# Optimization experiments

Hardware: AMD Instinct MI355X
Metric: run time of the kernel (lower is better)

The kernel has to match this reference:

```python
import jax, jax.numpy as jnp
import numpy as np

EPS = 1e-12  # F.normalize default eps


def setup_inputs() -> dict:
    key = jax.random.key(0)
    ks = jax.random.split(key, 8)
    b, c, h, w = 8, 192, 128, 128
    s = 0.02
    return {
        "x_in": jax.random.normal(ks[0], (b, c, h, w), dtype=jnp.float32),
        "w_split": jax.random.normal(ks[1], (c, c), dtype=jnp.float32) * s,
        "w_q": jax.random.normal(ks[2], (c, c), dtype=jnp.float32) * s,
        "w_k": jax.random.normal(ks[3], (c, c), dtype=jnp.float32) * s,
        "w_v": jax.random.normal(ks[4], (c, c), dtype=jnp.float32) * s,
        "w_proj": jax.random.normal(ks[5], (c, c), dtype=jnp.float32) * s,
        "b_proj": jax.random.normal(ks[6], (c,), dtype=jnp.float32) * s,
        "w_out": jax.random.normal(ks[7], (c, c), dtype=jnp.float32) * s,
    }


def _l2norm(x):
    # F.normalize(p=2, dim=-1): x / max(||x||, eps)
    n = jnp.sqrt(jnp.sum(x * x, axis=-1, keepdims=True))
    return x / jnp.maximum(n, EPS)


def reference(x_in, w_split, w_q, w_k, w_v, w_proj, b_proj, w_out):
    b, c, h, w = x_in.shape
    # conv_split0: 1x1 conv, no bias -> channel matmul
    x = jnp.einsum('oc,bchw->bohw', w_split, x_in)
    # [b,h,w,c] -> [b,hw,c]
    x = x.transpose(0, 2, 3, 1).reshape(b, h * w, c)
    # Linear: y = x @ W^T
    q = jnp.einsum('bnc,oc->bon', x, w_q)  # [b,c,hw] (already transposed)
    k = jnp.einsum('bnc,oc->bon', x, w_k)
    v = jnp.einsum('bnc,oc->bon', x, w_v)
    q = _l2norm(q)
    k = _l2norm(k)
    attn = jax.nn.softmax(jnp.einsum('bcn,bdn->bcd', k, q), axis=-1)  # [b,c,c]
    y = jnp.einsum('bcd,bdn->bcn', attn, v)  # [b,c,hw]
    y = y.transpose(0, 2, 1)  # [b,hw,c]
    out = jnp.einsum('bnc,oc->bno', y, w_proj) + b_proj
    out = out.reshape(b, h, w, c).transpose(0, 3, 1, 2)  # [b,c,h,w]
    out = jnp.einsum('oc,bchw->bohw', w_out, out)
    return out
```

## Files before the change

### kernel.cpp

```cpp
#include <hip/hip_runtime.h>


static constexpr int B_ = 8;
static constexpr int C_ = 192;
static constexpr int N_ = 16384;
static constexpr int CC2 = C_ * C_;
static constexpr int NCHUNK = 32;

using u16x8 = __attribute__((ext_vector_type(8))) unsigned short;
using bf16x8 = __attribute__((ext_vector_type(8))) __bf16;
using f32x4 = __attribute__((ext_vector_type(4))) float;

__device__ __forceinline__ unsigned short f2bf(float f) {
  unsigned int u = __builtin_bit_cast(unsigned int, f);
  u += 0x7FFFu + ((u >> 16) & 1u);
  return (unsigned short)(u >> 16);
}

__device__ __forceinline__ f32x4 mfma16(u16x8 a, u16x8 b, f32x4 c) {
  return __builtin_amdgcn_mfma_f32_16x16x32_bf16(
      __builtin_bit_cast(bf16x8, a), __builtin_bit_cast(bf16x8, b), c, 0, 0, 0);
}

__global__ void fold_kernel(const float* __restrict__ wsplit, const float* __restrict__ wq,
                            const float* __restrict__ wk, const float* __restrict__ wv,
                            const float* __restrict__ wproj, const float* __restrict__ bproj,
                            const float* __restrict__ wout,
                            float* __restrict__ Wq, float* __restrict__ WqT,
                            float* __restrict__ Wk, float* __restrict__ Wv,
                            float* __restrict__ Wo2, float* __restrict__ bias2) {
  int idx = blockIdx.x * 256 + threadIdx.x;
  if (idx < C_) {
    float s = 0.f;
    for (int c = 0; c < C_; ++c) s += wout[idx * C_ + c] * bproj[c];
    bias2[idx] = s;
  }
  if (idx >= 4 * CC2) return;
  int which = idx / CC2;
  int rem = idx % CC2;
  int o = rem / C_, c = rem % C_;
  const float* A = (which == 0) ? wq : (which == 1) ? wk : (which == 2) ? wv : wout;
  const float* Bm = (which == 3) ? wproj : wsplit;
  float s = 0.f;
  for (int e = 0; e < C_; ++e) s += A[o * C_ + e] * Bm[e * C_ + c];
  if (which == 0) { Wq[rem] = s; WqT[c * C_ + o] = s; }
  else if (which == 1) Wk[rem] = s;
  else if (which == 2) Wv[rem] = s;
  else Wo2[rem] = s;
}

template <bool ATOMIC>
__global__ __launch_bounds__(384) void gram3_kernel(const float* __restrict__ xin,
                                                    float* __restrict__ dst) {
  const int b = blockIdx.z, half = blockIdx.y, ch = blockIdx.x;
  const int k0 = ch * 512;
  __shared__ unsigned short Xs[2][C_][72];
  const int tid = threadIdx.x;
  const int wv = tid >> 6;
  const int lane = tid & 63;
  const int ln = lane & 15, mq = lane >> 4;
  const int arow0 = half * 96 + wv * 16;
  const int cbase = tid >> 4;
  const int k4 = tid & 15;
  const float* xb = xin + (size_t)b * C_ * N_;

  f32x4 acc[12];
#pragma unroll
  for (int j = 0; j < 12; ++j) acc[j] = (f32x4)0.0f;

  float4 ld[8];
  auto load_stage = [&](int kbase) {
#pragma unroll
    for (int j = 0; j < 8; ++j)
      ld[j] = *(const float4*)(xb + (size_t)(j * 24 + cbase) * N_ + kbase + k4 * 4);
  };
  auto write_stage = [&](int buf) {
#pragma unroll
    for (int j = 0; j < 8; ++j) {
      unsigned int lo = (unsigned)f2bf(ld[j].x) | ((unsigned)f2bf(ld[j].y) << 16);
      unsigned int hi = (unsigned)f2bf(ld[j].z) | ((unsigned)f2bf(ld[j].w) << 16);
      uint2 pk; pk.x = lo; pk.y = hi;
      *(uint2*)&Xs[buf][j * 24 + cbase][k4 * 4] = pk;
    }
  };

  load_stage(k0);
  write_stage(0);
  __syncthreads();
  for (int s = 0; s < 8; ++s) {
    if (s < 7) load_stage(k0 + (s + 1) * 64);
    const int cb = s & 1;
#pragma unroll
    for (int ks = 0; ks < 2; ++ks) {
      const int kk = ks * 32 + mq * 8;
      u16x8 a0 = *(const u16x8*)&Xs[cb][arow0 + ln][kk];
#pragma unroll
      for (int ct = 0; ct < 12; ++ct) {
        u16x8 bf = *(const u16x8*)&Xs[cb][ct * 16 + ln][kk];
        acc[ct] = mfma16(a0, bf, acc[ct]);
      }
    }
    if (s < 7) {
      write_stage(cb ^ 1);
      __syncthreads();
    }
  }
  float* out = ATOMIC ? dst + (size_t)b * CC2
                      : dst + ((size_t)b * NCHUNK + ch) * CC2;
#pragma unroll
  for (int ct = 0; ct < 12; ++ct)
#pragma unroll
    for (int r = 0; r < 4; ++r) {
      int row = arow0 + mq * 4 + r;
      int col = ct * 16 + ln;
      if (ATOMIC) atomicAdd(&out[row * C_ + col], acc[ct][r]);
      else out[row * C_ + col] = acc[ct][r];
    }
}

__global__ void gsum_kernel(const float* __restrict__ P, float* __restrict__ G) {
  const int j = (blockIdx.x * 256 + threadIdx.x) * 4;
  const int b = blockIdx.y;
  const float* base = P + (size_t)b * NCHUNK * CC2 + j;
  float4 s = {0.f, 0.f, 0.f, 0.f};
#pragma unroll
  for (int ch = 0; ch < NCHUNK; ++ch) {
    float4 v = *(const float4*)(base + (size_t)ch * CC2);
    s.x += v.x; s.y += v.y; s.z += v.z; s.w += v.w;
  }
  *(float4*)(G + (size_t)b * CC2 + j) = s;
}

__global__ __launch_bounds__(192) void tkqn_kernel(const float* __restrict__ Wk,
                                                   const float* __restrict__ Wq,
                                                   const float* __restrict__ G,
                                                   float* __restrict__ Tk,
                                                   float* __restrict__ qn) {
  const int b = blockIdx.y, d = blockIdx.x, t = threadIdx.x;
  const float* Gb = G + (size_t)b * CC2;
  float sk = 0.f, sq = 0.f;
  for (int c = 0; c < C_; ++c) {
    float g = Gb[c * C_ + t];
    sk += Wk[d * C_ + c] * g;
    sq += Wq[d * C_ + c] * g;
  }
  Tk[((size_t)b * C_ + d) * C_ + t] = sk;
  float val = sq * Wq[d * C_ + t];
  __shared__ float red[256];
  red[t] = val;
  if (t < 64) red[192 + t] = 0.f;
  __syncthreads();
  for (int st = 128; st > 0; st >>= 1) {
    if (t < st) red[t] += red[t + st];
    __syncthreads();
  }
  if (t == 0) qn[b * C_ + d] = fmaxf(sqrtf(fmaxf(red[0], 0.f)), 1e-12f);
}

__global__ __launch_bounds__(192) void attn_av_kernel(const float* __restrict__ Tk,
                                                      const float* __restrict__ WqT,
                                                      const float* __restrict__ Wk,
                                                      const float* __restrict__ Wv,
                                                      const float* __restrict__ qn,
                                                      float* __restrict__ Tv) {
  const int b = blockIdx.y, cc = blockIdx.x, t = threadIdx.x;
  __shared__ float tkrow[C_];
  __shared__ float arow[C_];
  __shared__ float red[256];
  tkrow[t] = Tk[((size_t)b * C_ + cc) * C_ + t];
  red[t] = tkrow[t] * Wk[cc * C_ + t];
  if (t < 64) red[192 + t] = 0.f;
  __syncthreads();
  for (int st = 128; st > 0; st >>= 1) {
    if (t < st) red[t] += red[t + st];
    __syncthreads();
  }
  float knv = fmaxf(sqrtf(fmaxf(red[0], 0.f)), 1e-12f);
  __syncthreads();
  float s = 0.f;
  for (int c = 0; c < C_; ++c) s += tkrow[c] * WqT[c * C_ + t];
  float lg = s / (knv * qn[b * C_ + t]);
  red[t] = lg;
  if (t < 64) red[192 + t] = -1e30f;
  __syncthreads();
  for (int st = 128; st > 0; st >>= 1) {
    if (t < st) red[t] = fmaxf(red[t], red[t + st]);
    __syncthreads();
  }
  float mx = red[0];
  __syncthreads();
  float e = expf(lg - mx);
  red[t] = e;
  if (t < 64) red[192 + t] = 0.f;
  __syncthreads();
  for (int st = 128; st > 0; st >>= 1) {
    if (t < st) red[t] += red[t + st];
    __syncthreads();
  }
  float a = e / red[0];
  arow[t] = a;
  __syncthreads();
  float sv = 0.f;
  for (int c = 0; c < C_; ++c) sv += arow[c] * Wv[c * C_ + t];
  Tv[((size_t)b * C_ + cc) * C_ + t] = sv;
}

__global__ void m_kernel(const float* __restrict__ Wo2, const float* __restrict__ Tv,
                         float* __restrict__ Mout) {
  int idx = blockIdx.x * 256 + threadIdx.x;
  if (idx >= B_ * CC2) return;
  int b = idx / CC2;
  int rc = idx % CC2;
  int i = rc / C_, j = rc % C_;
  float s = 0.f;
  for (int c = 0; c < C_; ++c) s += Wo2[i * C_ + c] * Tv[((size_t)b * C_ + c) * C_ + j];
  Mout[idx] = s;
}

__global__ __launch_bounds__(384) void final2_kernel(const float* __restrict__ xin,
                                                     const float* __restrict__ Mw,
                                                     const float* __restrict__ bias2,
                                                     float* __restrict__ out) {
  const int b = blockIdx.y;
  const int p0 = blockIdx.x * 128;
  __shared__ unsigned short Ts[128 * 192];
  const int tid = threadIdx.x;
  const int wv = tid >> 6;
  const int lane = tid & 63;
  const int ln = lane & 15, mq = lane >> 4;
  const float* Mb = Mw + (size_t)b * CC2;

  u16x8 afr[6][2];
  float bo[2][4];
#pragma unroll
  for (int i = 0; i < 2; ++i) {
    int row = 32 * wv + 16 * i + ln;
#pragma unroll
    for (int kc = 0; kc < 6; ++kc) {
      const float* src = Mb + row * C_ + kc * 32 + mq * 8;
      float4 u0 = *(const float4*)(src);
      float4 u1 = *(const float4*)(src + 4);
      u16x8 a;
      a[0] = f2bf(u0.x); a[1] = f2bf(u0.y); a[2] = f2bf(u0.z); a[3] = f2bf(u0.w);
      a[4] = f2bf(u1.x); a[5] = f2bf(u1.y); a[6] = f2bf(u1.z); a[7] = f2bf(u1.w);
      afr[kc][i] = a;
    }
#pragma unroll
    for (int r = 0; r < 4; ++r) bo[i][r] = bias2[32 * wv + 16 * i + mq * 4 + r];
  }

#pragma unroll
  for (int j = 0; j < 16; ++j) {
    int lin = j * 384 + tid;
    int c = lin >> 5, p4 = lin & 31;
    float4 v = *(const float4*)(xin + ((size_t)b * C_ + c) * N_ + p0 + p4 * 4);
#pragma unroll
    for (int jj = 0; jj < 4; ++jj) {
      int e = (jj + (p4 >> 1)) & 3;
      float val = (e == 0) ? v.x : (e == 1) ? v.y : (e == 2) ? v.z : v.w;
      int p = p4 * 4 + e;
      int idx = p * 192 + ((((c >> 3) ^ (p & 7)) << 3) | (c & 7));
      Ts[idx] = f2bf(val);
    }
  }
  __syncthreads();

#pragma unroll
  for (int pt = 0; pt < 8; ++pt) {
    const int p = pt * 16 + ln;
    f32x4 acc0 = (f32x4)0.0f, acc1 = (f32x4)0.0f;
#pragma unroll
    for (int kc = 0; kc < 6; ++kc) {
      u16x8 bf = *(const u16x8*)&Ts[p * 192 + (((kc * 4 + mq) ^ (p & 7)) << 3)];
      acc0 = mfma16(afr[kc][0], bf, acc0);
      acc1 = mfma16(afr[kc][1], bf, acc1);
    }
#pragma unroll
    for (int r = 0; r < 4; ++r) {
      int row0 = 32 * wv + mq * 4 + r;
      int row1 = row0 + 16;
      int pp = p0 + pt * 16 + ln;
      out[((size_t)b * C_ + row0) * N_ + pp] = acc0[r] + bo[0][r];
      out[((size_t)b * C_ + row1) * N_ + pp] = acc1[r] + bo[1][r];
    }
  }
}

extern "C" void kernel_launch(void* const* d_in, const int* in_sizes, int n_in,
                              void* d_out, int out_size, void* d_ws, size_t ws_size,
                              hipStream_t stream) {
  const float* xin    = (const float*)d_in[0];
  const float* wsplit = (const float*)d_in[1];
  const float* wq     = (const float*)d_in[2];
  const float* wk     = (const float*)d_in[3];
  const float* wv     = (const float*)d_in[4];
  const float* wproj  = (const float*)d_in[5];
  const float* bproj  = (const float*)d_in[6];
  const float* wout   = (const float*)d_in[7];
  float* out = (float*)d_out;

  float* ws = (float*)d_ws;
  float* G     = ws;
  float* Wq    = G + (size_t)B_ * CC2;
  float* WqT   = Wq + CC2;
  float* Wk    = WqT + CC2;
  float* Wv    = Wk + CC2;
  float* Wo2   = Wv + CC2;
  float* bias2 = Wo2 + CC2;
  float* Tk    = bias2 + 256;
  float* Tv    = Tk + (size_t)B_ * CC2;
  float* Mw    = Tv + (size_t)B_ * CC2;
  float* qn    = Mw + (size_t)B_ * CC2;
  float* P     = qn + 256 * B_;

  size_t base_floats = (size_t)(P - ws);
  size_t need_bytes = (base_floats + (size_t)B_ * NCHUNK * CC2) * sizeof(float);
  bool use_partials = ws_size >= need_bytes;

  fold_kernel<<<(4 * CC2 + 255) / 256, 256, 0, stream>>>(
      wsplit, wq, wk, wv, wproj, bproj, wout, Wq, WqT, Wk, Wv, Wo2, bias2);
  if (use_partials) {
    gram3_kernel<false><<<dim3(NCHUNK, 2, B_), 384, 0, stream>>>(xin, P);
    gsum_kernel<<<dim3(CC2 / 1024, B_), 256, 0, stream>>>(P, G);
  } else {
    hipMemsetAsync(G, 0, (size_t)B_ * CC2 * sizeof(float), stream);
    gram3_kernel<true><<<dim3(NCHUNK, 2, B_), 384, 0, stream>>>(xin, G);
  }
  tkqn_kernel<<<dim3(C_, B_), 192, 0, stream>>>(Wk, Wq, G, Tk, qn);
  attn_av_kernel<<<dim3(C_, B_), 192, 0, stream>>>(Tk, WqT, Wk, Wv, qn, Tv);
  m_kernel<<<(B_ * CC2 + 255) / 256, 256, 0, stream>>>(Wo2, Tv, Mw);
  final2_kernel<<<dim3(N_ / 128, B_), 384, 0, stream>>>(xin, Mw, bias2, out);
}
```

Before: 323.7 us.

## Merge small kernels, switch gram to 32x32 MFMA, pipeline final projection

The gram kernel now uses 32x32x16 MFMA with 192-thread blocks. The weight-fold work is merged into the partial-sum reduction kernel, and the three small attention kernels are fused into one cooperative kernel that uses grid syncs. The final kernel now processes four pixel tiles per block with double-buffered LDS so that global loads overlap MFMA work. The goal is to cut launch overhead and raise MFMA efficiency, at the cost of the grid-sync overhead and co-residency requirements of a 1536-block cooperative launch.

After: 644.9 us. 1.99x slower.

```diff
diff --git a/kernel.cpp b/kernel.cpp
--- a/kernel.cpp
+++ b/kernel.cpp
@@ -1,4 +1,8 @@
 #include <hip/hip_runtime.h>
+#include <hip/hip_bf16.h>
+#include <hip/hip_cooperative_groups.h>
+
+namespace cg = cooperative_groups;
 
 
 static constexpr int B_ = 8;
@@ -10,35 +14,129 @@
 using u16x8 = __attribute__((ext_vector_type(8))) unsigned short;
 using bf16x8 = __attribute__((ext_vector_type(8))) __bf16;
 using f32x4 = __attribute__((ext_vector_type(4))) float;
+using f32x16 = __attribute__((ext_vector_type(16))) float;
 
 __device__ __forceinline__ unsigned short f2bf(float f) {
   unsigned int u = __builtin_bit_cast(unsigned int, f);
   u += 0x7FFFu + ((u >> 16) & 1u);
   return (unsigned short)(u >> 16);
 }
-
+__device__ __forceinline__ unsigned int pk2bf(float x, float y) {
+  return (unsigned)f2bf(x) | ((unsigned)f2bf(y) << 16);
+}
 __device__ __forceinline__ f32x4 mfma16(u16x8 a, u16x8 b, f32x4 c) {
   return __builtin_amdgcn_mfma_f32_16x16x32_bf16(
       __builtin_bit_cast(bf16x8, a), __builtin_bit_cast(bf16x8, b), c, 0, 0, 0);
 }
-
-__global__ void fold_kernel(const float* __restrict__ wsplit, const float* __restrict__ wq,
-                            const float* __restrict__ wk, const float* __restrict__ wv,
-                            const float* __restrict__ wproj, const float* __restrict__ bproj,
-                            const float* __restrict__ wout,
-                            float* __restrict__ Wq, float* __restrict__ WqT,
-                            float* __restrict__ Wk, float* __restrict__ Wv,
-                            float* __restrict__ Wo2, float* __restrict__ bias2) {
-  int idx = blockIdx.x * 256 + threadIdx.x;
+__device__ __forceinline__ f32x16 mfma32(u16x8 a, u16x8 b, f32x16 c) {
+  return __builtin_amdgcn_mfma_f32_32x32x16_bf16(
+      __builtin_bit_cast(bf16x8, a), __builtin_bit_cast(bf16x8, b), c, 0, 0, 0);
+}
+
+template <bool PART>
+__global__ __launch_bounds__(192, 2) void gram4_kernel(const float* __restrict__ xin,
+                                                       float* __restrict__ dst) {
+  const int b = blockIdx.z, half = blockIdx.y, ch = blockIdx.x;
+  const int k0 = ch * 512;
+  __shared__ unsigned short Xs[2][C_][72];
+  const int tid = threadIdx.x;
+  const int wv = tid >> 6;
+  const int lane = tid & 63;
+  const int m32 = lane & 31;
+  const int hi = lane >> 5;
+  const int arow0 = half * 96 + wv * 32;
+  const int cth = tid >> 4;
+  const int k4 = tid & 15;
+  const float* xb = xin + (size_t)b * C_ * N_;
+
+  f32x16 acc[6];
+#pragma unroll
+  for (int j = 0; j < 6; ++j) acc[j] = (f32x16)0.0f;
+
+  float4 ld[16];
+  auto load_stage = [&](int kbase) {
+#pragma unroll
+    for (int j = 0; j < 16; ++j)
+      ld[j] = *(const float4*)(xb + (size_t)(j * 12 + cth) * N_ + kbase + k4 * 4);
+  };
+  auto write_stage = [&](int buf) {
+#pragma unroll
+    for (int j = 0; j < 16; ++j) {
+      uint2 pk;
+      pk.x = pk2bf(ld[j].x, ld[j].y);
+      pk.y = pk2bf(ld[j].z, ld[j].w);
+      *(uint2*)&Xs[buf][j * 12 + cth][k4 * 4] = pk;
+    }
+  };
+
+  load_stage(k0);
+  write_stage(0);
+  __syncthreads();
+  for (int s = 0; s < 8; ++s) {
+    if (s < 7) load_stage(k0 + (s + 1) * 64);
+    const int cb = s & 1;
+#pragma unroll
+    for (int ks = 0; ks < 4; ++ks) {
+      const int koff = ks * 16 + hi * 8;
+      u16x8 a = *(const u16x8*)&Xs[cb][arow0 + m32][koff];
+#pragma unroll
+      for (int ct = 0; ct < 6; ++ct) {
+        u16x8 bb = *(const u16x8*)&Xs[cb][ct * 32 + m32][koff];
+        acc[ct] = mfma32(a, bb, acc[ct]);
+      }
+    }
+    if (s < 7) {
+      write_stage(cb ^ 1);
+      __syncthreads();
+    }
+  }
+  float* outp = PART ? dst + ((size_t)b * NCHUNK + ch) * CC2
+                     : dst + (size_t)b * CC2;
+#pragma unroll
+  for (int ct = 0; ct < 6; ++ct)
+#pragma unroll
+    for (int reg = 0; reg < 16; ++reg) {
+      int row = arow0 + (reg & 3) + 8 * (reg >> 2) + 4 * hi;
+      int col = ct * 32 + m32;
+      if (PART) outp[row * C_ + col] = acc[ct][reg];
+      else atomicAdd(&outp[row * C_ + col], acc[ct][reg]);
+    }
+}
+
+__global__ void gsumfold_kernel(const float* __restrict__ P, float* __restrict__ G,
+                                const float* __restrict__ wsplit, const float* __restrict__ wq,
+                                const float* __restrict__ wk, const float* __restrict__ wv,
+                                const float* __restrict__ wproj, const float* __restrict__ bproj,
+                                const float* __restrict__ wout,
+                                float* __restrict__ Wq, float* __restrict__ WqT,
+                                float* __restrict__ Wk, float* __restrict__ Wv,
+                                float* __restrict__ Wo2, float* __restrict__ bias2,
+                                int do_gsum) {
+  const int gx = blockIdx.x, tid = threadIdx.x;
+  if (gx < 288) {
+    if (!do_gsum) return;
+    const int b = gx / 36, jb = gx % 36;
+    const int j = (jb * 256 + tid) * 4;
+    const float* base = P + (size_t)b * NCHUNK * CC2 + j;
+    float4 s = {0.f, 0.f, 0.f, 0.f};
+#pragma unroll
+    for (int ch = 0; ch < NCHUNK; ++ch) {
+      float4 v = *(const float4*)(base + (size_t)ch * CC2);
+      s.x += v.x; s.y += v.y; s.z += v.z; s.w += v.w;
+    }
+    *(float4*)(G + (size_t)b * CC2 + j) = s;
+    return;
+  }
+  const int idx = (gx - 288) * 256 + tid;
   if (idx < C_) {
     float s = 0.f;
     for (int c = 0; c < C_; ++c) s += wout[idx * C_ + c] * bproj[c];
     bias2[idx] = s;
   }
   if (idx >= 4 * CC2) return;
-  int which = idx / CC2;
-  int rem = idx % CC2;
-  int o = rem / C_, c = rem % C_;
+  const int which = idx / CC2;
+  const int rem = idx % CC2;
+  const int o = rem / C_, c = rem % C_;
   const float* A = (which == 0) ? wq : (which == 1) ? wk : (which == 2) ? wv : wout;
   const float* Bm = (which == 3) ? wproj : wsplit;
   float s = 0.f;
@@ -49,186 +147,83 @@
   else Wo2[rem] = s;
 }
 
-template <bool ATOMIC>
-__global__ __launch_bounds__(384) void gram3_kernel(const float* __restrict__ xin,
-                                                    float* __restrict__ dst) {
-  const int b = blockIdx.z, half = blockIdx.y, ch = blockIdx.x;
-  const int k0 = ch * 512;
-  __shared__ unsigned short Xs[2][C_][72];
-  const int tid = threadIdx.x;
-  const int wv = tid >> 6;
-  const int lane = tid & 63;
-  const int ln = lane & 15, mq = lane >> 4;
-  const int arow0 = half * 96 + wv * 16;
-  const int cbase = tid >> 4;
-  const int k4 = tid & 15;
-  const float* xb = xin + (size_t)b * C_ * N_;
-
-  f32x4 acc[12];
-#pragma unroll
-  for (int j = 0; j < 12; ++j) acc[j] = (f32x4)0.0f;
-
-  float4 ld[8];
-  auto load_stage = [&](int kbase) {
-#pragma unroll
-    for (int j = 0; j < 8; ++j)
-      ld[j] = *(const float4*)(xb + (size_t)(j * 24 + cbase) * N_ + kbase + k4 * 4);
-  };
-  auto write_stage = [&](int buf) {
-#pragma unroll
-    for (int j = 0; j < 8; ++j) {
-      unsigned int lo = (unsigned)f2bf(ld[j].x) | ((unsigned)f2bf(ld[j].y) << 16);
-      unsigned int hi = (unsigned)f2bf(ld[j].z) | ((unsigned)f2bf(ld[j].w) << 16);
-      uint2 pk; pk.x = lo; pk.y = hi;
-      *(uint2*)&Xs[buf][j * 24 + cbase][k4 * 4] = pk;
-    }
-  };
-
-  load_stage(k0);
-  write_stage(0);
-  __syncthreads();
-  for (int s = 0; s < 8; ++s) {
-    if (s < 7) load_stage(k0 + (s + 1) * 64);
-    const int cb = s & 1;
-#pragma unroll
-    for (int ks = 0; ks < 2; ++ks) {
-      const int kk = ks * 32 + mq * 8;
-      u16x8 a0 = *(const u16x8*)&Xs[cb][arow0 + ln][kk];
-#pragma unroll
-      for (int ct = 0; ct < 12; ++ct) {
-        u16x8 bf = *(const u16x8*)&Xs[cb][ct * 16 + ln][kk];
-        acc[ct] = mfma16(a0, bf, acc[ct]);
-      }
-    }
-    if (s < 7) {
-      write_stage(cb ^ 1);
-      __syncthreads();
-    }
-  }
-  float* out = ATOMIC ? dst + (size_t)b * CC2
-                      : dst + ((size_t)b * NCHUNK + ch) * CC2;
-#pragma unroll
-  for (int ct = 0; ct < 12; ++ct)
-#pragma unroll
-    for (int r = 0; r < 4; ++r) {
-      int row = arow0 + mq * 4 + r;
-      int col = ct * 16 + ln;
-      if (ATOMIC) atomicAdd(&out[row * C_ + col], acc[ct][r]);
-      else out[row * C_ + col] = acc[ct][r];
-    }
-}
-
-__global__ void gsum_kernel(const float* __restrict__ P, float* __restrict__ G) {
-  const int j = (blockIdx.x * 256 + threadIdx.x) * 4;
-  const int b = blockIdx.y;
-  const float* base = P + (size_t)b * NCHUNK * CC2 + j;
-  float4 s = {0.f, 0.f, 0.f, 0.f};
-#pragma unroll
-  for (int ch = 0; ch < NCHUNK; ++ch) {
-    float4 v = *(const float4*)(base + (size_t)ch * CC2);
-    s.x += v.x; s.y += v.y; s.z += v.z; s.w += v.w;
-  }
-  *(float4*)(G + (size_t)b * CC2 + j) = s;
-}
-
-__global__ __launch_bounds__(192) void tkqn_kernel(const float* __restrict__ Wk,
-                                                   const float* __restrict__ Wq,
-                                                   const float* __restrict__ G,
-                                                   float* __restrict__ Tk,
-                                                   float* __restrict__ qn) {
-  const int b = blockIdx.y, d = blockIdx.x, t = threadIdx.x;
+__device__ __forceinline__ float block_sum192(float v, float* wred, int t) {
+#pragma unroll
+  for (int off = 32; off > 0; off >>= 1) v += __shfl_down(v, off);
+  if ((t & 63) == 0) wred[t >> 6] = v;
+  __syncthreads();
+  float r = wred[0] + wred[1] + wred[2];
+  __syncthreads();
+  return r;
+}
+__device__ __forceinline__ float block_max192(float v, float* wred, int t) {
+#pragma unroll
+  for (int off = 32; off > 0; off >>= 1) v = fmaxf(v, __shfl_down(v, off));
+  if ((t & 63) == 0) wred[t >> 6] = v;
+  __syncthreads();
+  float r = fmaxf(fmaxf(wred[0], wred[1]), wred[2]);
+  __syncthreads();
+  return r;
+}
+
+__global__ __launch_bounds__(192) void mid_kernel(const float* __restrict__ G,
+                                                  const float* __restrict__ Wq,
+                                                  const float* __restrict__ WqT,
+                                                  const float* __restrict__ Wk,
+                                                  const float* __restrict__ Wv,
+                                                  const float* __restrict__ Wo2,
+                                                  float* __restrict__ qn,
+                                                  float* __restrict__ Tv,
+                                                  float* __restrict__ Mw) {
+  cg::grid_group grid = cg::this_grid();
+  const int b = blockIdx.y, r = blockIdx.x, t = threadIdx.x;
   const float* Gb = G + (size_t)b * CC2;
-  float sk = 0.f, sq = 0.f;
-  for (int c = 0; c < C_; ++c) {
-    float g = Gb[c * C_ + t];
-    sk += Wk[d * C_ + c] * g;
-    sq += Wq[d * C_ + c] * g;
-  }
-  Tk[((size_t)b * C_ + d) * C_ + t] = sk;
-  float val = sq * Wq[d * C_ + t];
-  __shared__ float red[256];
-  red[t] = val;
-  if (t < 64) red[192 + t] = 0.f;
-  __syncthreads();
-  for (int st = 128; st > 0; st >>= 1) {
-    if (t < st) red[t] += red[t + st];
-    __syncthreads();
-  }
-  if (t == 0) qn[b * C_ + d] = fmaxf(sqrtf(fmaxf(red[0], 0.f)), 1e-12f);
-}
-
-__global__ __launch_bounds__(192) void attn_av_kernel(const float* __restrict__ Tk,
-                                                      const float* __restrict__ WqT,
-                                                      const float* __restrict__ Wk,
-                                                      const float* __restrict__ Wv,
-                                                      const float* __restrict__ qn,
-                                                      float* __restrict__ Tv) {
-  const int b = blockIdx.y, cc = blockIdx.x, t = threadIdx.x;
-  __shared__ float tkrow[C_];
-  __shared__ float arow[C_];
-  __shared__ float red[256];
-  tkrow[t] = Tk[((size_t)b * C_ + cc) * C_ + t];
-  red[t] = tkrow[t] * Wk[cc * C_ + t];
-  if (t < 64) red[192 + t] = 0.f;
-  __syncthreads();
-  for (int st = 128; st > 0; st >>= 1) {
-    if (t < st) red[t] += red[t + st];
-    __syncthreads();
-  }
-  float knv = fmaxf(sqrtf(fmaxf(red[0], 0.f)), 1e-12f);
-  __syncthreads();
-  float s = 0.f;
-  for (int c = 0; c < C_; ++c) s += tkrow[c] * WqT[c * C_ + t];
-  float lg = s / (knv * qn[b * C_ + t]);
-  red[t] = lg;
-  if (t < 64) red[192 + t] = -1e30f;
-  __syncthreads();
-  for (int st = 128; st > 0; st >>= 1) {
-    if (t < st) red[t] = fmaxf(red[t], red[t + st]);
-    __syncthreads();
-  }
-  float mx = red[0];
-  __syncthreads();
+  __shared__ float sh[C_];
+  __shared__ float wred[4];
+
+  float sq = 0.f;
+  for (int c = 0; c < C_; ++c) sq += Wq[r * C_ + c] * Gb[c * C_ + t];
+  float tot = block_sum192(sq * Wq[r * C_ + t], wred, t);
+  if (t == 0) qn[b * C_ + r] = fmaxf(sqrtf(fmaxf(tot, 0.f)), 1e-12f);
+  grid.sync();
+
+  float tk = 0.f;
+  for (int c = 0; c < C_; ++c) tk += Wk[r * C_ + c] * Gb[c * C_ + t];
+  sh[t] = tk;
+  float kn2 = block_sum192(tk * Wk[r * C_ + t], wred, t);
+  float knv = fmaxf(sqrtf(fmaxf(kn2, 0.f)), 1e-12f);
+  float lg = 0.f;
+  for (int c = 0; c < C_; ++c) lg += sh[c] * WqT[c * C_ + t];
+  lg /= (knv * qn[b * C_ + t]);
+  float mx = block_max192(lg, wred, t);
   float e = expf(lg - mx);
-  red[t] = e;
-  if (t < 64) red[192 + t] = 0.f;
-  __syncthreads();
-  for (int st = 128; st > 0; st >>= 1) {
-    if (t < st) red[t] += red[t + st];
-    __syncthreads();
-  }
-  float a = e / red[0];
-  arow[t] = a;
+  float se = block_sum192(e, wred, t);
+  float a = e / se;
+  sh[t] = a;
   __syncthreads();
   float sv = 0.f;
-  for (int c = 0; c < C_; ++c) sv += arow[c] * Wv[c * C_ + t];
-  Tv[((size_t)b * C_ + cc) * C_ + t] = sv;
-}
-
-__global__ void m_kernel(const float* __restrict__ Wo2, const float* __restrict__ Tv,
-                         float* __restrict__ Mout) {
-  int idx = blockIdx.x * 256 + threadIdx.x;
-  if (idx >= B_ * CC2) return;
-  int b = idx / CC2;
-  int rc = idx % CC2;
-  int i = rc / C_, j = rc % C_;
-  float s = 0.f;
-  for (int c = 0; c < C_; ++c) s += Wo2[i * C_ + c] * Tv[((size_t)b * C_ + c) * C_ + j];
-  Mout[idx] = s;
-}
-
-__global__ __launch_bounds__(384) void final2_kernel(const float* __restrict__ xin,
+  for (int c = 0; c < C_; ++c) sv += sh[c] * Wv[c * C_ + t];
+  Tv[((size_t)b * C_ + r) * C_ + t] = sv;
+  grid.sync();
+
+  float sm = 0.f;
+  for (int c = 0; c < C_; ++c) sm += Wo2[r * C_ + c] * Tv[((size_t)b * C_ + c) * C_ + t];
+  Mw[((size_t)b * C_ + r) * C_ + t] = sm;
+}
+
+__global__ __launch_bounds__(384) void final3_kernel(const float* __restrict__ xin,
                                                      const float* __restrict__ Mw,
                                                      const float* __restrict__ bias2,
                                                      float* __restrict__ out) {
-  const int b = blockIdx.y;
-  const int p0 = blockIdx.x * 128;
-  __shared__ unsigned short Ts[128 * 192];
+  const int beta = blockIdx.x;
+  const int b = beta >> 5, q = beta & 31;
+  __shared__ unsigned short Ts[2][128 * 192];
   const int tid = threadIdx.x;
   const int wv = tid >> 6;
   const int lane = tid & 63;
   const int ln = lane & 15, mq = lane >> 4;
   const float* Mb = Mw + (size_t)b * CC2;
+  const float* xb = xin + (size_t)b * C_ * N_;
 
   u16x8 afr[6][2];
   float bo[2][4];
@@ -249,39 +244,56 @@
     for (int r = 0; r < 4; ++r) bo[i][r] = bias2[32 * wv + 16 * i + mq * 4 + r];
   }
 
-#pragma unroll
-  for (int j = 0; j < 16; ++j) {
-    int lin = j * 384 + tid;
-    int c = lin >> 5, p4 = lin & 31;
-    float4 v = *(const float4*)(xin + ((size_t)b * C_ + c) * N_ + p0 + p4 * 4);
-#pragma unroll
-    for (int jj = 0; jj < 4; ++jj) {
-      int e = (jj + (p4 >> 1)) & 3;
-      float val = (e == 0) ? v.x : (e == 1) ? v.y : (e == 2) ? v.z : v.w;
-      int p = p4 * 4 + e;
-      int idx = p * 192 + ((((c >> 3) ^ (p & 7)) << 3) | (c & 7));
-      Ts[idx] = f2bf(val);
-    }
-  }
-  __syncthreads();
-
-#pragma unroll
-  for (int pt = 0; pt < 8; ++pt) {
-    const int p = pt * 16 + ln;
-    f32x4 acc0 = (f32x4)0.0f, acc1 = (f32x4)0.0f;
-#pragma unroll
-    for (int kc = 0; kc < 6; ++kc) {
-      u16x8 bf = *(const u16x8*)&Ts[p * 192 + (((kc * 4 + mq) ^ (p & 7)) << 3)];
-      acc0 = mfma16(afr[kc][0], bf, acc0);
-      acc1 = mfma16(afr[kc][1], bf, acc1);
-    }
-#pragma unroll
-    for (int r = 0; r < 4; ++r) {
-      int row0 = 32 * wv + mq * 4 + r;
-      int row1 = row0 + 16;
-      int pp = p0 + pt * 16 + ln;
-      out[((size_t)b * C_ + row0) * N_ + pp] = acc0[r] + bo[0][r];
-      out[((size_t)b * C_ + row1) * N_ + pp] = acc1[r] + bo[1][r];
+  float4 ld[16];
+  auto load_tile = [&](int it) {
+    const int p0 = (q * 4 + it) * 128;
+#pragma unroll
+    for (int j = 0; j < 16; ++j) {
+      int lin = j * 384 + tid;
+      int c = lin >> 5, p4 = lin & 31;
+      ld[j] = *(const float4*)(xb + (size_t)c * N_ + p0 + p4 * 4);
+    }
+  };
+  auto stage = [&](int buf) {
+#pragma unroll
+    for (int j = 0; j < 16; ++j) {
+      int lin = j * 384 + tid;
+      int c = lin >> 5, p4 = lin & 31;
+#pragma unroll
+      for (int jj = 0; jj < 4; ++jj) {
+        int e = (jj + (p4 >> 1)) & 3;
+        float val = (e == 0) ? ld[j].x : (e == 1) ? ld[j].y : (e == 2) ? ld[j].z : ld[j].w;
+        int p = p4 * 4 + e;
+        Ts[buf][p * 192 + ((((c >> 3) ^ (p & 7)) << 3) | (c & 7))] = f2bf(val);
+      }
+    }
+  };
+
+  load_tile(0);
+  for (int it = 0; it < 4; ++it) {
+    const int bf = it & 1;
+    stage(bf);
+    __syncthreads();
+    if (it < 3) load_tile(it + 1);
+    const int p0 = (q * 4 + it) * 128;
+#pragma unroll
+    for (int pt = 0; pt < 8; ++pt) {
+      const int p = pt * 16 + ln;
+      f32x4 acc0 = (f32x4)0.0f, acc1 = (f32x4)0.0f;
+#pragma unroll
+      for (int kc = 0; kc < 6; ++kc) {
+        u16x8 bfr = *(const u16x8*)&Ts[bf][p * 192 + (((kc * 4 + mq) ^ (p & 7)) << 3)];
+        acc0 = mfma16(afr[kc][0], bfr, acc0);
+        acc1 = mfma16(afr[kc][1], bfr, acc1);
+      }
+#pragma unroll
+      for (int r = 0; r < 4; ++r) {
+        int row0 = 32 * wv + mq * 4 + r;
+        int row1 = row0 + 16;
+        int pp = p0 + pt * 16 + ln;
+        out[((size_t)b * C_ + row0) * N_ + pp] = acc0[r] + bo[0][r];
+        out[((size_t)b * C_ + row1) * N_ + pp] = acc1[r] + bo[1][r];
+      }
     }
   }
 }
@@ -307,27 +319,28 @@
   float* Wv    = Wk + CC2;
   float* Wo2   = Wv + CC2;
   float* bias2 = Wo2 + CC2;
-  float* Tk    = bias2 + 256;
-  float* Tv    = Tk + (size_t)B_ * CC2;
+  float* Tv    = bias2 + 256;
   float* Mw    = Tv + (size_t)B_ * CC2;
   float* qn    = Mw + (size_t)B_ * CC2;
   float* P     = qn + 256 * B_;
 
   size_t base_floats = (size_t)(P - ws);
   size_t need_bytes = (base_floats + (size_t)B_ * NCHUNK * CC2) * sizeof(float);
-  bool use_partials = ws_size >= need_bytes;
-
-  fold_kernel<<<(4 * CC2 + 255) / 256, 256, 0, stream>>>(
-      wsplit, wq, wk, wv, wproj, bproj, wout, Wq, WqT, Wk, Wv, Wo2, bias2);
+  int use_partials = ws_size >= need_bytes ? 1 : 0;
+
   if (use_partials) {
-    gram3_kernel<false><<<dim3(NCHUNK, 2, B_), 384, 0, stream>>>(xin, P);
-    gsum_kernel<<<dim3(CC2 / 1024, B_), 256, 0, stream>>>(P, G);
+    gram4_kernel<true><<<dim3(NCHUNK, 2, B_), 192, 0, stream>>>(xin, P);
   } else {
     hipMemsetAsync(G, 0, (size_t)B_ * CC2 * sizeof(float), stream);
-    gram3_kernel<true><<<dim3(NCHUNK, 2, B_), 384, 0, stream>>>(xin, G);
-  }
-  tkqn_kernel<<<dim3(C_, B_), 192, 0, stream>>>(Wk, Wq, G, Tk, qn);
-  attn_av_kernel<<<dim3(C_, B_), 192, 0, stream>>>(Tk, WqT, Wk, Wv, qn, Tv);
-  m_kernel<<<(B_ * CC2 + 255) / 256, 256, 0, stream>>>(Wo2, Tv, Mw);
-  final2_kernel<<<dim3(N_ / 128, B_), 384, 0, stream>>>(xin, Mw, bias2, out);
-}
+    gram4_kernel<false><<<dim3(NCHUNK, 2, B_), 192, 0, stream>>>(xin, G);
+  }
+  gsumfold_kernel<<<288 + 576, 256, 0, stream>>>(P, G, wsplit, wq, wk, wv, wproj, bproj,
+                                                 wout, Wq, WqT, Wk, Wv, Wo2, bias2,
+                                                 use_partials);
+  {
+    void* args[] = {(void*)&G, (void*)&Wq, (void*)&WqT, (void*)&Wk, (void*)&Wv,
+                    (void*)&Wo2, (void*)&qn, (void*)&Tv, (void*)&Mw};
+    hipLaunchCooperativeKernel((void*)mid_kernel, dim3(C_, B_), dim3(192), args, 0, stream);
+  }
+  final3_kernel<<<256, 384, 0, stream>>>(xin, Mw, bias2, out);
+}
```
